# Kernel optimization log

Hardware: AMD Instinct MI355X
Metric: run time of the kernel (lower is better)

Reference implementation:

```python
import jax, jax.numpy as jnp
import numpy as np

N = 100000
IN_DIM = 256
HID = 64
HEADS = 2
OUT_DIM = 64
E = 1600000
NEG_SLOPE = 0.2


def gat_conv(x, edge_index, W, att_src, att_dst, bias):
    # PyG GATConv with heads=HEADS, concat=True, add_self_loops=True.
    # x: [N, IN_DIM]; edge_index: [2, E] (row0=src, row1=dst)
    loops = jnp.arange(N, dtype=edge_index.dtype)
    src = jnp.concatenate([edge_index[0], loops])  # [E+N]
    dst = jnp.concatenate([edge_index[1], loops])  # [E+N]
    h = (x @ W).reshape(N, HEADS, HID)             # [N, H, C]
    a_src = jnp.einsum('nhc,hc->nh', h, att_src)   # [N, H]
    a_dst = jnp.einsum('nhc,hc->nh', h, att_dst)   # [N, H]
    e = jax.nn.leaky_relu(a_src[src] + a_dst[dst], NEG_SLOPE)  # [E+N, H]
    # segment softmax over incoming edges of each dst node
    m = jax.ops.segment_max(e, dst, num_segments=N)            # [N, H]
    p = jnp.exp(e - m[dst])
    denom = jax.ops.segment_sum(p, dst, num_segments=N)        # [N, H]
    alpha = p / denom[dst]                                     # [E+N, H]
    msg = h[src] * alpha[:, :, None]                           # [E+N, H, C]
    out = jax.ops.segment_sum(msg, dst, num_segments=N)        # [N, H, C]
    return out.reshape(N, HEADS * HID) + bias


def setup_inputs() -> dict:
    key = jax.random.key(0)
    ks = jax.random.split(key, 12)
    s_in = 1.0 / np.sqrt(IN_DIM)
    s_h = 1.0 / np.sqrt(HID)
    s_fc = 1.0 / np.sqrt(HEADS * HID * 2)
    return {
        'x': jax.random.normal(ks[0], (N, IN_DIM), jnp.float32),
        'edge_index_connected': jax.random.randint(ks[1], (2, E), 0, N, jnp.int32),
        'edge_index_liked': jax.random.randint(ks[2], (2, E), 0, N, jnp.int32),
        'W1': jax.random.normal(ks[3], (IN_DIM, HEADS * HID), jnp.float32) * s_in,
        'att_src1': jax.random.normal(ks[4], (HEADS, HID), jnp.float32) * s_h,
        'att_dst1': jax.random.normal(ks[5], (HEADS, HID), jnp.float32) * s_h,
        'b1': jnp.zeros((HEADS * HID,), jnp.float32),
        'W2': jax.random.normal(ks[6], (IN_DIM, HEADS * HID), jnp.float32) * s_in,
        'att_src2': jax.random.normal(ks[7], (HEADS, HID), jnp.float32) * s_h,
        'att_dst2': jax.random.normal(ks[8], (HEADS, HID), jnp.float32) * s_h,
        'b2': jnp.zeros((HEADS * HID,), jnp.float32),
        'fc_W': jax.random.normal(ks[9], (HEADS * HID * 2, OUT_DIM), jnp.float32) * s_fc,
        'fc_b': jnp.zeros((OUT_DIM,), jnp.float32),
    }


def reference(x, edge_index_connected, edge_index_liked, W1, att_src1, att_dst1, b1,
              W2, att_src2, att_dst2, b2, fc_W, fc_b):
    xc = jax.nn.relu(gat_conv(x, edge_index_connected, W1, att_src1, att_dst1, b1))
    xl = jax.nn.relu(gat_conv(x, edge_index_liked, W2, att_src2, att_dst2, b2))
    x_comb = jnp.concatenate([xc, xl], axis=1)  # [N, 4*HID]
    return x_comb @ fc_W + fc_b
```

## Files before the change

### kernel.cpp

```cpp
#include <hip/hip_runtime.h>
#include <hip/hip_fp16.h>
#include <math.h>

#define NN 100000
#define IN_DIM 256
#define HCH 128
#define OUT_DIM 64
#define EE 1600000
#define NEG_SLOPE 0.2f

#define NB 1024
#define NPB 98
#define CAP 2048

#define GEMM_BLOCKS 1563
#define CONV_BLOCKS 320
#define BUCKET_PER_LAYER 512
#define SORT_BLOCKS (2 * NB)

typedef _Float16 half8v __attribute__((ext_vector_type(8)));
typedef _Float16 half4v __attribute__((ext_vector_type(4)));
typedef __fp16 fp16x2 __attribute__((ext_vector_type(2)));
typedef float float4v __attribute__((ext_vector_type(4)));
typedef unsigned int u32;

union H2U { u32 u; fp16x2 h; };

__device__ __forceinline__ float lrelu(float v) { return v > 0.f ? v : NEG_SLOPE * v; }

__global__ __launch_bounds__(256, 8) void prep_kernel(
    const float* __restrict__ W0, const float* __restrict__ W1,
    const float* __restrict__ fcW,
    _Float16* __restrict__ wt, _Float16* __restrict__ fcw2,
    const int* __restrict__ ei0, const int* __restrict__ ei1,
    int* __restrict__ gcursor, int* __restrict__ bstore)
{
    __shared__ int hist[NB];
    __shared__ int base[NB];
    const int tid = threadIdx.x;

    if (blockIdx.x < CONV_BLOCKS) {
        int i = blockIdx.x * 256 + tid;
        if (i < 2 * IN_DIM * HCH) {
            int l = i >> 15, rem = i & 32767;
            int c = rem >> 8, k = rem & 255;
            const float* W = l ? W1 : W0;
            wt[i] = (_Float16)W[(size_t)k * HCH + c];
            return;
        }
        int j = i - 2 * IN_DIM * HCH;
        if (j < 256 * OUT_DIM) {
            int c = j >> 8, k = j & 255;
            fcw2[j] = (_Float16)fcW[(size_t)k * OUT_DIM + c];
        }
        return;
    }

    const int bb = blockIdx.x - CONV_BLOCKS;
    const int lay = bb >> 9;
    const int idx = bb & 511;
    const int* src = lay ? ei1 : ei0;
    const int* dst = src + EE;
    int* gcur = gcursor + lay * NB;
    int* bst = bstore + (size_t)lay * NB * CAP;

    const int per = (EE + BUCKET_PER_LAYER - 1) / BUCKET_PER_LAYER;
    const int e0 = idx * per;
    const int e1 = min(EE, e0 + per);
    for (int i = tid; i < NB; i += 256) hist[i] = 0;
    __syncthreads();
    for (int i = e0 + tid; i < e1; i += 256)
        atomicAdd(&hist[dst[i] / NPB], 1);
    __syncthreads();
    for (int b = tid; b < NB; b += 256) {
        int c = hist[b];
        base[b] = c ? atomicAdd(&gcur[b], c) : 0;
        hist[b] = 0;
    }
    __syncthreads();
    for (int i = e0 + tid; i < e1; i += 256) {
        int d = dst[i];
        int s = src[i];
        int b = d / NPB;
        int pos = base[b] + atomicAdd(&hist[b], 1);
        if (pos >= 0 && pos < CAP) bst[b * CAP + pos] = (s << 7) | (d - b * NPB);
    }
}

__global__ __launch_bounds__(256, 3) void mid_kernel(
    const float* __restrict__ x, const _Float16* __restrict__ wt,
    const float* __restrict__ attS0, const float* __restrict__ attD0,
    const float* __restrict__ attS1, const float* __restrict__ attD1,
    _Float16* __restrict__ h16, float* __restrict__ a_s, float* __restrict__ a_d,
    const int* __restrict__ gcursor, int* __restrict__ bstore,
    int* __restrict__ gstart, int* __restrict__ gend, int n)
{
    __shared__ __align__(16) _Float16 smem[64 * 72 + 256 * 72];
    __shared__ float attv[4][128];
    const int tid = threadIdx.x;

    const long long TS = SORT_BLOCKS;
    const long long TB = GEMM_BLOCKS + SORT_BLOCKS;
    const int k = blockIdx.x;
    const int slo = (int)(((long long)k * TS) / TB);
    const int shi = (int)(((long long)(k + 1) * TS) / TB);

    if (shi > slo) {
        int* raw = (int*)smem;
        int* sorted = raw + CAP;
        int* curs = sorted + CAP;
        int* scanbuf = curs + 128;
        const int sb = slo;
        const int lay = sb >> 10;
        const int b = sb & (NB - 1);
        const int* gcur = gcursor + lay * NB;
        int* bst = bstore + (size_t)lay * NB * CAP;
        int* gs = gstart + (size_t)lay * NN;
        int* ge = gend + (size_t)lay * NN;

        const int node0 = b * NPB;
        const int nnode = min(NPB, n - node0);
        if (nnode <= 0) return;
        int cnt = gcur[b];
        cnt = cnt < 0 ? 0 : (cnt > CAP ? CAP : cnt);

        for (int i = tid; i < cnt; i += 256) raw[i] = bst[b * CAP + i];
        if (tid < 128) curs[tid] = 0;
        __syncthreads();
        for (int i = tid; i < cnt; i += 256) atomicAdd(&curs[raw[i] & 127], 1);
        __syncthreads();
        if (tid < 128) scanbuf[tid] = curs[tid];
        __syncthreads();
        for (int off = 1; off < 128; off <<= 1) {
            int v = 0;
            if (tid < 128) { v = scanbuf[tid]; if (tid >= off) v += scanbuf[tid - off]; }
            __syncthreads();
            if (tid < 128) scanbuf[tid] = v;
            __syncthreads();
        }
        if (tid < 128) {
            int ex = tid ? scanbuf[tid - 1] : 0;
            curs[tid] = ex;
            if (tid < nnode) {
                gs[node0 + tid] = b * CAP + ex;
                ge[node0 + tid] = b * CAP + scanbuf[tid];
            }
        }
        __syncthreads();
        for (int i = tid; i < cnt; i += 256) {
            int item = raw[i];
            int pos = atomicAdd(&curs[item & 127], 1);
            if (pos >= 0 && pos < CAP) sorted[pos] = item >> 7;
        }
        __syncthreads();
        for (int i = tid; i < cnt; i += 256) bst[b * CAP + i] = sorted[i];
        return;
    }

    _Float16 (*As)[72] = (_Float16(*)[72])smem;
    _Float16 (*Bs)[72] = (_Float16(*)[72])(smem + 64 * 72);
    const int gb = k - slo;
    const int lane = tid & 63, wave = tid >> 6;
    const int wm = wave & 1, wn = wave >> 1;
    const int q = lane >> 4, r16 = lane & 15;
    const int row0 = gb * 64;

    if (tid < 128) {
        attv[0][tid] = attS0[tid]; attv[1][tid] = attD0[tid];
        attv[2][tid] = attS1[tid]; attv[3][tid] = attD1[tid];
    }

    float4v acc[2][8];
#pragma unroll
    for (int i = 0; i < 2; ++i)
#pragma unroll
        for (int j = 0; j < 8; ++j) acc[i][j] = (float4v){0.f, 0.f, 0.f, 0.f};

    const int ar = tid >> 2, aq = tid & 3;
    const bool rok = (row0 + ar) < n;
    for (int kt = 0; kt < IN_DIM; kt += 64) {
        const float* xp = x + (size_t)(row0 + ar) * IN_DIM + kt + aq * 16;
#pragma unroll
        for (int i = 0; i < 4; ++i) {
            float4 v = rok ? *(const float4*)(xp + i * 4) : make_float4(0.f, 0.f, 0.f, 0.f);
            half4v hv = { (_Float16)v.x, (_Float16)v.y, (_Float16)v.z, (_Float16)v.w };
            *(half4v*)&As[ar][aq * 16 + i * 4] = hv;
        }
        const _Float16* wp = wt + (size_t)tid * IN_DIM + kt;
#pragma unroll
        for (int i = 0; i < 8; ++i)
            *(half8v*)&Bs[tid][i * 8] = *(const half8v*)(wp + i * 8);
        __syncthreads();
#pragma unroll
        for (int s = 0; s < 2; ++s) {
            half8v af[2], bf[8];
#pragma unroll
            for (int t = 0; t < 2; ++t)
                af[t] = *(half8v*)&As[wm * 32 + t * 16 + r16][s * 32 + q * 8];
#pragma unroll
            for (int t = 0; t < 8; ++t)
                bf[t] = *(half8v*)&Bs[wn * 128 + t * 16 + r16][s * 32 + q * 8];
#pragma unroll
            for (int mt = 0; mt < 2; ++mt)
#pragma unroll
                for (int nt = 0; nt < 8; ++nt)
                    acc[mt][nt] = __builtin_amdgcn_mfma_f32_16x16x32_f16(
                        af[mt], bf[nt], acc[mt][nt], 0, 0, 0);
        }
        __syncthreads();
    }
    _Float16 (*eb)[264] = (_Float16(*)[264])smem;
#pragma unroll
    for (int mt = 0; mt < 2; ++mt) {
        const int er = wm * 32 + mt * 16 + q * 4;
#pragma unroll
        for (int reg = 0; reg < 4; ++reg)
#pragma unroll
            for (int nt = 0; nt < 8; ++nt)
                eb[er + reg][wn * 128 + nt * 16 + r16] = (_Float16)acc[mt][nt][reg];
    }
    __syncthreads();
    const int r = tid >> 2, qq = tid & 3;
    const int grow = row0 + r;
    if (grow < n) {
        const int l2 = qq >> 1;
        const int hh = qq & 1;
        const float* avS = &attv[l2 * 2 + 0][hh * 64];
        const float* avD = &attv[l2 * 2 + 1][hh * 64];
        _Float16* hout = h16 + (size_t)l2 * NN * HCH + (size_t)grow * HCH + hh * 64;
        float ds = 0.f, dd = 0.f;
#pragma unroll
        for (int i = 0; i < 8; ++i) {
            half8v v = *(half8v*)&eb[r][qq * 64 + i * 8];
            *(half8v*)(hout + i * 8) = v;
#pragma unroll
            for (int j = 0; j < 8; ++j) {
                float f = (float)v[j];
                ds = fmaf(f, avS[i * 8 + j], ds);
                dd = fmaf(f, avD[i * 8 + j], dd);
            }
        }
        a_s[(size_t)l2 * 2 * NN + 2 * grow + hh] = ds;
        a_d[(size_t)l2 * 2 * NN + 2 * grow + hh] = dd;
    }
}

__global__ __launch_bounds__(256) void agg_fc(
    const _Float16* __restrict__ h16, const float2* __restrict__ a_s,
    const float2* __restrict__ a_d, const int* __restrict__ gstart,
    const int* __restrict__ gend, const int* __restrict__ bstore,
    const float* __restrict__ bias0, const float* __restrict__ bias1,
    const _Float16* __restrict__ fw2, const float* __restrict__ fcb,
    float* __restrict__ out, int n)
{
    __shared__ __align__(16) uint2 sh[4][64];
    __shared__ __align__(16) _Float16 xcs[16][264];
    const int tid = threadIdx.x;
    const int wid = tid >> 6, lane = tid & 63;
    const int wbase = blockIdx.x * 16 + wid * 4;
    const int cl = lane & 15;
    const int w2 = lane >> 4;
    const int hh = cl >> 3;
    const u32 psel = hh ? 0x07060302u : 0x05040100u;
    const fp16x2 one2 = { (__fp16)1.f, (__fp16)1.f };

    float bv[2][8];
#pragma unroll
    for (int j = 0; j < 8; ++j) {
        bv[0][j] = bias0[cl * 8 + j];
        bv[1][j] = bias1[cl * 8 + j];
    }

    for (int ni = 0; ni < 4; ++ni) {
        const int node = wbase + ni;
        const bool valid = node < n;
        const int nn = valid ? node : 0;
        const int xr = wid * 4 + ni;
        for (int lay = 0; lay < 2; ++lay) {
            const _Float16* hL = h16 + (size_t)lay * NN * HCH;
            const float2* asL = a_s + (size_t)lay * NN;
            const float2* adL = a_d + (size_t)lay * NN;
            const int* ssort = bstore + (size_t)lay * NB * CAP;
            int start = gstart[(size_t)lay * NN + nn];
            int end = gend[(size_t)lay * NN + nn];
            start = start < 0 ? 0 : (start > NB * CAP ? NB * CAP : start);
            end = end < start ? start : (end > NB * CAP ? NB * CAP : end);
            const float2 ad = adL[nn];
            const float2 asn = asL[nn];

            float acc[8] = {0.f, 0.f, 0.f, 0.f, 0.f, 0.f, 0.f, 0.f};
            float den = 0.f;

            for (int base2 = start; base2 < end; base2 += 64) {
                const int j = base2 + lane;
                const int cnt = min(64, end - base2);
                float p0 = 0.f, p1 = 0.f;
                int s = 0;
                if (j < end) {
                    s = ssort[j];
                    if ((unsigned)s >= (unsigned)n) s = 0;
                    float2 a = asL[s];
                    p0 = __expf(lrelu(a.x + ad.x));
                    p1 = __expf(lrelu(a.y + ad.y));
                }
                H2U pk; pk.h = __builtin_amdgcn_cvt_pkrtz(p0, p1);
                sh[wid][lane] = make_uint2((u32)s, pk.u);
                __builtin_amdgcn_wave_barrier();
                const int cnt8 = (cnt + 7) & ~7;
                for (int t = 0; t < cnt8; t += 8) {
                    const uint4 rec = *(const uint4*)&sh[wid][t + 2 * w2];
                    H2U pph; pph.u = __builtin_amdgcn_perm(rec.w, rec.y, psel);
                    const half8v hv0 = *(const half8v*)(hL + ((rec.x << 7) | (u32)(cl << 3)));
                    const half8v hv1 = *(const half8v*)(hL + ((rec.z << 7) | (u32)(cl << 3)));
                    const u32* ap = (const u32*)&hv0;
                    const u32* bp = (const u32*)&hv1;
#pragma unroll
                    for (int d2 = 0; d2 < 4; ++d2) {
                        H2U pe, po;
                        pe.u = __builtin_amdgcn_perm(bp[d2], ap[d2], 0x05040100u);
                        po.u = __builtin_amdgcn_perm(bp[d2], ap[d2], 0x07060302u);
                        acc[2 * d2]     = __builtin_amdgcn_fdot2(pe.h, pph.h, acc[2 * d2], false);
                        acc[2 * d2 + 1] = __builtin_amdgcn_fdot2(po.h, pph.h, acc[2 * d2 + 1], false);
                    }
                    den = __builtin_amdgcn_fdot2(pph.h, one2, den, false);
                }
                __builtin_amdgcn_wave_barrier();
            }
            const float ps0 = __expf(lrelu(asn.x + ad.x));
            const float ps1 = __expf(lrelu(asn.y + ad.y));
            if (w2 == 0) {
                const half8v hv = *(const half8v*)(hL + (((u32)nn << 7) | (u32)(cl << 3)));
                const float pl = hh ? ps1 : ps0;
#pragma unroll
                for (int j2 = 0; j2 < 8; ++j2)
                    acc[j2] = fmaf(pl, (float)hv[j2], acc[j2]);
                den += pl;
            }
#pragma unroll
            for (int j2 = 0; j2 < 8; ++j2) {
                acc[j2] += __shfl_xor(acc[j2], 16, 64);
                acc[j2] += __shfl_xor(acc[j2], 32, 64);
            }
            den += __shfl_xor(den, 16, 64);
            den += __shfl_xor(den, 32, 64);
            if (lane < 16) {
                const float inv = 1.f / den;
                half8v o;
#pragma unroll
                for (int j2 = 0; j2 < 8; ++j2)
                    o[j2] = (_Float16)fmaxf(acc[j2] * inv + bv[lay][j2], 0.f);
                *(half8v*)&xcs[xr][lay * HCH + cl * 8] = o;
            }
        }
    }
    __syncthreads();

    const int q = lane >> 4, r16 = lane & 15;
    float4v facc = (float4v){0.f, 0.f, 0.f, 0.f};
#pragma unroll
    for (int s = 0; s < 8; ++s) {
        const half8v af = *(half8v*)&xcs[r16][s * 32 + q * 8];
        const half8v bf =
            *(const half8v*)(fw2 + (size_t)(wid * 16 + r16) * 256 + s * 32 + q * 8);
        facc = __builtin_amdgcn_mfma_f32_16x16x32_f16(af, bf, facc, 0, 0, 0);
    }
    const int col = wid * 16 + r16;
    const float fb = fcb[col];
#pragma unroll
    for (int reg = 0; reg < 4; ++reg) {
        const int grow = blockIdx.x * 16 + q * 4 + reg;
        if (grow < n)
            out[(size_t)grow * OUT_DIM + col] = facc[reg] + fb;
    }
}

extern "C" void kernel_launch(void* const* d_in, const int* in_sizes, int n_in,
                              void* d_out, int out_size, void* d_ws, size_t ws_size,
                              hipStream_t stream)
{
    const float* x = (const float*)d_in[0];
    const int* ei[2] = { (const int*)d_in[1], (const int*)d_in[2] };
    const float* W[2] = { (const float*)d_in[3], (const float*)d_in[7] };
    const float* attS[2] = { (const float*)d_in[4], (const float*)d_in[8] };
    const float* attD[2] = { (const float*)d_in[5], (const float*)d_in[9] };
    const float* bias[2] = { (const float*)d_in[6], (const float*)d_in[10] };
    const float* fcW = (const float*)d_in[11];
    const float* fcb = (const float*)d_in[12];
    float* out = (float*)d_out;

    char* p = (char*)d_ws;
    size_t need = 0;
    auto carve = [&](size_t bytes) {
        char* r = p;
        size_t b = (bytes + 255) & ~(size_t)255;
        p += b;
        need += b;
        return r;
    };
    _Float16* h16 = (_Float16*)carve((size_t)2 * NN * HCH * 2);
    _Float16* wt = (_Float16*)carve((size_t)2 * IN_DIM * HCH * 2);
    _Float16* fcw2 = (_Float16*)carve((size_t)256 * OUT_DIM * 2);
    float* a_s = (float*)carve((size_t)2 * NN * 8);
    float* a_d = (float*)carve((size_t)2 * NN * 8);
    int* gcursor = (int*)carve((size_t)2 * NB * 4);
    int* bstore = (int*)carve((size_t)2 * NB * CAP * 4);
    int* gstart = (int*)carve((size_t)2 * NN * 4);
    int* gend = (int*)carve((size_t)2 * NN * 4);
    if (need > ws_size) return;

    (void)hipMemsetAsync(gcursor, 0, (size_t)2 * NB * 4, stream);

    prep_kernel<<<CONV_BLOCKS + 2 * BUCKET_PER_LAYER, 256, 0, stream>>>(
        W[0], W[1], fcW, wt, fcw2, ei[0], ei[1], gcursor, bstore);

    mid_kernel<<<GEMM_BLOCKS + SORT_BLOCKS, 256, 0, stream>>>(
        x, wt, attS[0], attD[0], attS[1], attD[1],
        h16, a_s, a_d, gcursor, bstore, gstart, gend, NN);

    agg_fc<<<(NN + 15) / 16, 256, 0, stream>>>(
        h16, (const float2*)a_s, (const float2*)a_d,
        gstart, gend, bstore, bias[0], bias[1], fcw2, fcb, out, NN);
}
```

Before: 478.7 us.

## Split fused aggregation+FC into per-layer aggregation grid and separate MFMA FC kernel

The fused agg_fc kernel is split into two kernels. agg_kernel puts the two GAT layers on grid.y and maps four nodes per wave, one per 16-lane group, in place of one node per wave looping over 64-edge chunks. It writes the fp16 concatenated activations to a new workspace buffer. A separate fc_mfma kernel then does the final linear layer, 64 rows per block with four MFMA column tiles per wave. The aim is better parallelism and less lane waste on low-degree nodes, at the cost of an extra kernel launch and a round trip of the intermediate through global memory.

```diff
diff --git a/kernel.cpp b/kernel.cpp
--- a/kernel.cpp
+++ b/kernel.cpp
@@ -245,132 +245,148 @@
     }
 }
 
-__global__ __launch_bounds__(256) void agg_fc(
+__global__ __launch_bounds__(256) void agg_kernel(
     const _Float16* __restrict__ h16, const float2* __restrict__ a_s,
     const float2* __restrict__ a_d, const int* __restrict__ gstart,
     const int* __restrict__ gend, const int* __restrict__ bstore,
     const float* __restrict__ bias0, const float* __restrict__ bias1,
-    const _Float16* __restrict__ fw2, const float* __restrict__ fcb,
-    float* __restrict__ out, int n)
+    _Float16* __restrict__ xc16, int n)
 {
     __shared__ __align__(16) uint2 sh[4][64];
-    __shared__ __align__(16) _Float16 xcs[16][264];
-    const int tid = threadIdx.x;
-    const int wid = tid >> 6, lane = tid & 63;
-    const int wbase = blockIdx.x * 16 + wid * 4;
-    const int cl = lane & 15;
-    const int w2 = lane >> 4;
-    const int hh = cl >> 3;
+    const int lay = blockIdx.y;
+    const _Float16* hL = h16 + (size_t)lay * NN * HCH;
+    const float2* asL = a_s + (size_t)lay * NN;
+    const float2* adL = a_d + (size_t)lay * NN;
+    const int* gsL = gstart + (size_t)lay * NN;
+    const int* geL = gend + (size_t)lay * NN;
+    const int* ssort = bstore + (size_t)lay * NB * CAP;
+    const float* bias = lay ? bias1 : bias0;
+
+    const int wid = threadIdx.x >> 6, lane = threadIdx.x & 63;
+    const int g = lane >> 4;
+    const int i = lane & 15;
+    const int hh = i >> 3;
     const u32 psel = hh ? 0x07060302u : 0x05040100u;
     const fp16x2 one2 = { (__fp16)1.f, (__fp16)1.f };
 
-    float bv[2][8];
-#pragma unroll
-    for (int j = 0; j < 8; ++j) {
-        bv[0][j] = bias0[cl * 8 + j];
-        bv[1][j] = bias1[cl * 8 + j];
-    }
-
-    for (int ni = 0; ni < 4; ++ni) {
-        const int node = wbase + ni;
-        const bool valid = node < n;
-        const int nn = valid ? node : 0;
-        const int xr = wid * 4 + ni;
-        for (int lay = 0; lay < 2; ++lay) {
-            const _Float16* hL = h16 + (size_t)lay * NN * HCH;
-            const float2* asL = a_s + (size_t)lay * NN;
-            const float2* adL = a_d + (size_t)lay * NN;
-            const int* ssort = bstore + (size_t)lay * NB * CAP;
-            int start = gstart[(size_t)lay * NN + nn];
-            int end = gend[(size_t)lay * NN + nn];
-            start = start < 0 ? 0 : (start > NB * CAP ? NB * CAP : start);
-            end = end < start ? start : (end > NB * CAP ? NB * CAP : end);
-            const float2 ad = adL[nn];
-            const float2 asn = asL[nn];
-
-            float acc[8] = {0.f, 0.f, 0.f, 0.f, 0.f, 0.f, 0.f, 0.f};
-            float den = 0.f;
-
-            for (int base2 = start; base2 < end; base2 += 64) {
-                const int j = base2 + lane;
-                const int cnt = min(64, end - base2);
-                float p0 = 0.f, p1 = 0.f;
-                int s = 0;
-                if (j < end) {
-                    s = ssort[j];
-                    if ((unsigned)s >= (unsigned)n) s = 0;
-                    float2 a = asL[s];
-                    p0 = __expf(lrelu(a.x + ad.x));
-                    p1 = __expf(lrelu(a.y + ad.y));
-                }
-                H2U pk; pk.h = __builtin_amdgcn_cvt_pkrtz(p0, p1);
-                sh[wid][lane] = make_uint2((u32)s, pk.u);
-                __builtin_amdgcn_wave_barrier();
-                const int cnt8 = (cnt + 7) & ~7;
-                for (int t = 0; t < cnt8; t += 8) {
-                    const uint4 rec = *(const uint4*)&sh[wid][t + 2 * w2];
-                    H2U pph; pph.u = __builtin_amdgcn_perm(rec.w, rec.y, psel);
-                    const half8v hv0 = *(const half8v*)(hL + ((rec.x << 7) | (u32)(cl << 3)));
-                    const half8v hv1 = *(const half8v*)(hL + ((rec.z << 7) | (u32)(cl << 3)));
-                    const u32* ap = (const u32*)&hv0;
-                    const u32* bp = (const u32*)&hv1;
-#pragma unroll
-                    for (int d2 = 0; d2 < 4; ++d2) {
-                        H2U pe, po;
-                        pe.u = __builtin_amdgcn_perm(bp[d2], ap[d2], 0x05040100u);
-                        po.u = __builtin_amdgcn_perm(bp[d2], ap[d2], 0x07060302u);
-                        acc[2 * d2]     = __builtin_amdgcn_fdot2(pe.h, pph.h, acc[2 * d2], false);
-                        acc[2 * d2 + 1] = __builtin_amdgcn_fdot2(po.h, pph.h, acc[2 * d2 + 1], false);
-                    }
-                    den = __builtin_amdgcn_fdot2(pph.h, one2, den, false);
-                }
-                __builtin_amdgcn_wave_barrier();
+    const int node = blockIdx.x * 16 + wid * 4 + g;
+    const bool valid = node < n;
+    const int nn = valid ? node : 0;
+
+    float bv[8];
+#pragma unroll
+    for (int j = 0; j < 8; ++j) bv[j] = bias[i * 8 + j];
+
+    int start = gsL[nn], end = geL[nn];
+    start = start < 0 ? 0 : (start > NB * CAP ? NB * CAP : start);
+    end = end < start ? start : (end > NB * CAP ? NB * CAP : end);
+    const int cnt = end - start;
+    const float2 ad = adL[nn];
+    const float2 asn = asL[nn];
+
+    float acc[8] = {0.f, 0.f, 0.f, 0.f, 0.f, 0.f, 0.f, 0.f};
+    float den = 0.f;
+    uint2* slots = &sh[wid][g * 16];
+
+    for (int base = 0; base < cnt; base += 16) {
+        const int idx = start + base + i;
+        float p0 = 0.f, p1 = 0.f;
+        int s = 0;
+        if (idx < end) {
+            s = ssort[idx];
+            if ((unsigned)s >= (unsigned)n) s = 0;
+            float2 a = asL[s];
+            p0 = __expf(lrelu(a.x + ad.x));
+            p1 = __expf(lrelu(a.y + ad.y));
+        }
+        H2U pk; pk.h = __builtin_amdgcn_cvt_pkrtz(p0, p1);
+        slots[i] = make_uint2((u32)s, pk.u);
+        __builtin_amdgcn_wave_barrier();
+        const int c2 = min(16, cnt - base);
+        for (int t = 0; t < c2; t += 2) {
+            const uint4 rec = *(const uint4*)&slots[t];
+            H2U pph; pph.u = __builtin_amdgcn_perm(rec.w, rec.y, psel);
+            const half8v hv0 = *(const half8v*)(hL + ((rec.x << 7) | (u32)(i << 3)));
+            const half8v hv1 = *(const half8v*)(hL + ((rec.z << 7) | (u32)(i << 3)));
+            const u32* ap = (const u32*)&hv0;
+            const u32* bp = (const u32*)&hv1;
+#pragma unroll
+            for (int d2 = 0; d2 < 4; ++d2) {
+                H2U pe, po;
+                pe.u = __builtin_amdgcn_perm(bp[d2], ap[d2], 0x05040100u);
+                po.u = __builtin_amdgcn_perm(bp[d2], ap[d2], 0x07060302u);
+                acc[2 * d2]     = __builtin_amdgcn_fdot2(pe.h, pph.h, acc[2 * d2], false);
+                acc[2 * d2 + 1] = __builtin_amdgcn_fdot2(po.h, pph.h, acc[2 * d2 + 1], false);
             }
-            const float ps0 = __expf(lrelu(asn.x + ad.x));
-            const float ps1 = __expf(lrelu(asn.y + ad.y));
-            if (w2 == 0) {
-                const half8v hv = *(const half8v*)(hL + (((u32)nn << 7) | (u32)(cl << 3)));
-                const float pl = hh ? ps1 : ps0;
-#pragma unroll
-                for (int j2 = 0; j2 < 8; ++j2)
-                    acc[j2] = fmaf(pl, (float)hv[j2], acc[j2]);
-                den += pl;
-            }
-#pragma unroll
-            for (int j2 = 0; j2 < 8; ++j2) {
-                acc[j2] += __shfl_xor(acc[j2], 16, 64);
-                acc[j2] += __shfl_xor(acc[j2], 32, 64);
-            }
-            den += __shfl_xor(den, 16, 64);
-            den += __shfl_xor(den, 32, 64);
-            if (lane < 16) {
-                const float inv = 1.f / den;
-                half8v o;
-#pragma unroll
-                for (int j2 = 0; j2 < 8; ++j2)
-                    o[j2] = (_Float16)fmaxf(acc[j2] * inv + bv[lay][j2], 0.f);
-                *(half8v*)&xcs[xr][lay * HCH + cl * 8] = o;
-            }
-        }
+            den = __builtin_amdgcn_fdot2(pph.h, one2, den, false);
+        }
+        __builtin_amdgcn_wave_barrier();
+    }
+    {
+        const float ps0 = __expf(lrelu(asn.x + ad.x));
+        const float ps1 = __expf(lrelu(asn.y + ad.y));
+        const half8v hv = *(const half8v*)(hL + (((u32)nn << 7) | (u32)(i << 3)));
+        const float pl = hh ? ps1 : ps0;
+#pragma unroll
+        for (int j2 = 0; j2 < 8; ++j2)
+            acc[j2] = fmaf(pl, (float)hv[j2], acc[j2]);
+        den += pl;
+    }
+    if (valid) {
+        const float inv = 1.f / den;
+        half8v o;
+#pragma unroll
+        for (int j2 = 0; j2 < 8; ++j2)
+            o[j2] = (_Float16)fmaxf(acc[j2] * inv + bv[j2], 0.f);
+        *(half8v*)(xc16 + (size_t)node * 256 + lay * HCH + i * 8) = o;
+    }
+}
+
+__global__ __launch_bounds__(256) void fc_mfma(const _Float16* __restrict__ xc16,
+                                               const _Float16* __restrict__ fw2,
+                                               const float* __restrict__ fcb,
+                                               float* __restrict__ out, int n)
+{
+    __shared__ _Float16 axs[64][264];
+    const int tid = threadIdx.x;
+    const int lane = tid & 63, wave = tid >> 6;
+    const int q = lane >> 4, r16 = lane & 15;
+    const int row0 = blockIdx.x * 64;
+
+#pragma unroll
+    for (int i = 0; i < 8; ++i) {
+        const int idx = i * 256 + tid;
+        const int row = idx >> 5;
+        const int kg = (idx & 31) * 8;
+        half8v v = { 0, 0, 0, 0, 0, 0, 0, 0 };
+        if (row0 + row < n)
+            v = *(const half8v*)(xc16 + (size_t)(row0 + row) * 256 + kg);
+        *(half8v*)&axs[row][kg] = v;
     }
     __syncthreads();
 
-    const int q = lane >> 4, r16 = lane & 15;
-    float4v facc = (float4v){0.f, 0.f, 0.f, 0.f};
+    float4v acc[4];
+#pragma unroll
+    for (int i = 0; i < 4; ++i) acc[i] = (float4v){0.f, 0.f, 0.f, 0.f};
 #pragma unroll
     for (int s = 0; s < 8; ++s) {
-        const half8v af = *(half8v*)&xcs[r16][s * 32 + q * 8];
-        const half8v bf =
-            *(const half8v*)(fw2 + (size_t)(wid * 16 + r16) * 256 + s * 32 + q * 8);
-        facc = __builtin_amdgcn_mfma_f32_16x16x32_f16(af, bf, facc, 0, 0, 0);
-    }
-    const int col = wid * 16 + r16;
-    const float fb = fcb[col];
-#pragma unroll
-    for (int reg = 0; reg < 4; ++reg) {
-        const int grow = blockIdx.x * 16 + q * 4 + reg;
-        if (grow < n)
-            out[(size_t)grow * OUT_DIM + col] = facc[reg] + fb;
+        const half8v af = *(half8v*)&axs[wave * 16 + r16][s * 32 + q * 8];
+#pragma unroll
+        for (int nt = 0; nt < 4; ++nt) {
+            const half8v bf =
+                *(const half8v*)(fw2 + (size_t)(nt * 16 + r16) * 256 + s * 32 + q * 8);
+            acc[nt] = __builtin_amdgcn_mfma_f32_16x16x32_f16(af, bf, acc[nt], 0, 0, 0);
+        }
+    }
+#pragma unroll
+    for (int nt = 0; nt < 4; ++nt) {
+        const int col = nt * 16 + r16;
+#pragma unroll
+        for (int reg = 0; reg < 4; ++reg) {
+            const int row = row0 + wave * 16 + q * 4 + reg;
+            if (row < n)
+                out[(size_t)row * OUT_DIM + col] = acc[nt][reg] + fcb[col];
+        }
     }
 }
 
@@ -398,6 +414,7 @@
         return r;
     };
     _Float16* h16 = (_Float16*)carve((size_t)2 * NN * HCH * 2);
+    _Float16* xc16 = (_Float16*)carve((size_t)NN * 256 * 2);
     _Float16* wt = (_Float16*)carve((size_t)2 * IN_DIM * HCH * 2);
     _Float16* fcw2 = (_Float16*)carve((size_t)256 * OUT_DIM * 2);
     float* a_s = (float*)carve((size_t)2 * NN * 8);
@@ -417,7 +434,9 @@
         x, wt, attS[0], attD[0], attS[1], attD[1],
         h16, a_s, a_d, gcursor, bstore, gstart, gend, NN);
 
-    agg_fc<<<(NN + 15) / 16, 256, 0, stream>>>(
+    agg_kernel<<<dim3((NN + 15) / 16, 2), 256, 0, stream>>>(
         h16, (const float2*)a_s, (const float2*)a_d,
-        gstart, gend, bstore, bias[0], bias[1], fcw2, fcb, out, NN);
+        gstart, gend, bstore, bias[0], bias[1], xc16, NN);
+
+    fc_mfma<<<GEMM_BLOCKS, 256, 0, stream>>>(xc16, fcw2, fcb, out, NN);
 }
```

Result: faster. 468.6 us (-2.1%).
